# Kernel tuning notes

Measured on AMD Instinct MI355X. Metric: run time of the kernel, lower is better.

The kernel has to match this reference:

```python
import jax, jax.numpy as jnp
import numpy as np

B, T, D_MODEL = 2, 2048, 2048
NUM_HEADS, NUM_KV_HEADS, HEAD_DIM = 16, 16, 128
NUM_Q_HEADS = 2 * NUM_HEADS  # diff-v2 doubles the query heads


def _rope_freqs(seqlen, dim_half, base=10000.0):
    inv = 1.0 / (base ** (np.arange(0, dim_half, dtype=np.float32) / dim_half))
    t = np.arange(seqlen, dtype=np.float32)
    ang = np.outer(t, inv)  # [T, dim_half]
    return jnp.asarray(np.cos(ang)), jnp.asarray(np.sin(ang))


def apply_rotary_interleaved(x, cos, sin):
    # x: [B, T, H, D]; cos/sin: [T, D//2]; pairs are adjacent (interleaved=True)
    x1, x2 = x[..., 0::2], x[..., 1::2]
    c = cos[None, :, None, :]
    s = sin[None, :, None, :]
    o1 = x1 * c - x2 * s
    o2 = x1 * s + x2 * c
    return jnp.stack([o1, o2], axis=-1).reshape(x.shape)


def setup_inputs() -> dict:
    key = jax.random.key(0)
    ks = jax.random.split(key, 6)
    x = jax.random.normal(ks[0], (B, T, D_MODEL), dtype=jnp.float32)
    cos, sin = _rope_freqs(T, HEAD_DIM // 2)
    sc = 1.0 / np.sqrt(D_MODEL)
    Wq = jax.random.normal(ks[1], (D_MODEL, NUM_Q_HEADS * HEAD_DIM), dtype=jnp.float32) * sc
    Wk = jax.random.normal(ks[2], (D_MODEL, NUM_KV_HEADS * HEAD_DIM), dtype=jnp.float32) * sc
    Wv = jax.random.normal(ks[3], (D_MODEL, NUM_KV_HEADS * HEAD_DIM), dtype=jnp.float32) * sc
    Wo = jax.random.normal(ks[4], (NUM_HEADS * HEAD_DIM, D_MODEL), dtype=jnp.float32) * sc
    Wlam = jax.random.normal(ks[5], (D_MODEL, NUM_HEADS), dtype=jnp.float32) * sc
    return {"x": x, "cos": cos, "sin": sin, "Wq": Wq, "Wk": Wk, "Wv": Wv, "Wo": Wo, "Wlam": Wlam}


def reference(x, cos, sin, Wq, Wk, Wv, Wo, Wlam):
    b, t, _ = x.shape
    q = (x @ Wq).reshape(b, t, NUM_Q_HEADS, HEAD_DIM)
    k = (x @ Wk).reshape(b, t, NUM_KV_HEADS, HEAD_DIM)
    v = (x @ Wv).reshape(b, t, NUM_KV_HEADS, HEAD_DIM)
    q = apply_rotary_interleaved(q, cos, sin)
    k = apply_rotary_interleaved(k, cos, sin)
    # GQA: repeat kv heads to match the doubled query heads
    rep = NUM_Q_HEADS // NUM_KV_HEADS
    k = jnp.repeat(k, rep, axis=2)
    v = jnp.repeat(v, rep, axis=2)
    scale = 1.0 / np.sqrt(HEAD_DIM)
    scores = jnp.einsum('bthd,bshd->bhts', q, k) * scale  # [B, 2H, T, T]
    causal = jnp.tril(jnp.ones((t, t), dtype=bool))
    scores = jnp.where(causal[None, None], scores, jnp.finfo(scores.dtype).min)
    p = jax.nn.softmax(scores, axis=-1)
    attn = jnp.einsum('bhts,bshd->bthd', p, v)  # [B, T, 2H, D]
    lam = jax.nn.sigmoid(x @ Wlam)  # [B, T, H]
    attn1, attn2 = attn[:, :, 0::2], attn[:, :, 1::2]
    out = attn1 - lam[..., None] * attn2  # [B, T, H, D]
    return out.reshape(b, t, NUM_HEADS * HEAD_DIM) @ Wo
```

## Files before the change

kernel.cpp:

```cpp
#include <hip/hip_runtime.h>

#define T_SEQ 2048
#define BATCH 2
#define DMODEL 2048
#define NQH 32
#define NKVH 16
#define HD 128

typedef _Float16 f16;
typedef _Float16 f16x8 __attribute__((ext_vector_type(8)));
typedef _Float16 f16x4 __attribute__((ext_vector_type(4)));
typedef _Float16 f16x2 __attribute__((ext_vector_type(2)));
typedef float f32x4 __attribute__((ext_vector_type(4)));

typedef const __attribute__((address_space(1))) void* gptr_t;
typedef __attribute__((address_space(3))) void* sptr_t;
#define GLDS16(g, l) __builtin_amdgcn_global_load_lds((gptr_t)(g), (sptr_t)(l), 16, 0, 0)

__global__ __launch_bounds__(256) void k_transpose_all(const float* __restrict__ Wq,
                                                       const float* __restrict__ Wk,
                                                       const float* __restrict__ Wv,
                                                       const float* __restrict__ Wo,
                                                       f16* __restrict__ WqkvT,
                                                       f16* __restrict__ WoT) {
  __shared__ float tile[32][33];
  const int z = blockIdx.z;
  const float* W;
  f16* WT;
  int N;
  if (z == 0)      { W = Wq; WT = WqkvT;                          N = 4096; }
  else if (z == 1) { W = Wk; WT = WqkvT + (size_t)4096 * 2048;    N = 2048; }
  else if (z == 2) { W = Wv; WT = WqkvT + (size_t)6144 * 2048;    N = 2048; }
  else             { W = Wo; WT = WoT;                            N = 2048; }
  const int K = 2048;
  int n0 = blockIdx.x * 32;
  if (n0 >= N) return;
  int k0 = blockIdx.y * 32;
  int tx = threadIdx.x & 31;
  int ty0 = threadIdx.x >> 5;
  #pragma unroll
  for (int i = 0; i < 4; ++i) {
    int ty = ty0 + i * 8;
    tile[ty][tx] = W[(size_t)(k0 + ty) * N + n0 + tx];
  }
  __syncthreads();
  #pragma unroll
  for (int i = 0; i < 4; ++i) {
    int ty = ty0 + i * 8;
    WT[(size_t)(n0 + ty) * K + k0 + tx] = (f16)tile[tx][ty];
  }
}

template<int BM, int BN, int WM, int WN, int OM>
__global__ __launch_bounds__(512, 2) void k_gemm2(const f16* __restrict__ A,
                                                  const f16* __restrict__ BT,
                                                  void* __restrict__ C0,
                                                  f16* __restrict__ Kh,
                                                  f16* __restrict__ VTg,
                                                  const float* __restrict__ cosb,
                                                  const float* __restrict__ sinb,
                                                  int M, int N, int K) {
  constexpr int MR = BM / WM / 16;
  constexpr int NR = BN / WN / 16;
  constexpr int ACH = BM / 64;
  constexpr int BCH = BN / 64;
  __shared__ alignas(16) f16 Al[2][BM * 64];
  __shared__ alignas(16) f16 Bl[2][BN * 64];
  const int tid = threadIdx.x;
  const int lane = tid & 63;
  const int w = tid >> 6;
  const int wr = w / WN, wc = w % WN;
  const int lr = lane & 15, lg = lane >> 4;
  const int nbx = N / BN;
  const int cpx = gridDim.x >> 3;
  const int wg = (blockIdx.x & 7) * cpx + (blockIdx.x >> 3);
  const int m0 = (wg / nbx) * BM, n0 = (wg % nbx) * BN;

  auto STAGE = [&](int buf, int kk) {
    #pragma unroll
    for (int q = 0; q < ACH; ++q) {
      int idx = q * 512 + tid;
      int r = idx >> 3, g = idx & 7;
      GLDS16(A + (size_t)(m0 + r) * K + kk + ((g ^ (r & 7)) * 8), &Al[buf][idx * 8]);
    }
    #pragma unroll
    for (int q = 0; q < BCH; ++q) {
      int idx = q * 512 + tid;
      int r = idx >> 3, g = idx & 7;
      GLDS16(BT + (size_t)(n0 + r) * K + kk + ((g ^ (r & 7)) * 8), &Bl[buf][idx * 8]);
    }
  };

  f32x4 acc[MR][NR] = {};
  STAGE(0, 0);
  const int nt = K / 64;
  #pragma unroll 2
  for (int t = 0; t < nt; ++t) {
    const int buf = t & 1;
    if (t + 1 < nt) {
      STAGE(buf ^ 1, (t + 1) * 64);
      __builtin_amdgcn_sched_barrier(0);
      if constexpr (ACH + BCH == 8) asm volatile("s_waitcnt vmcnt(8)" ::: "memory");
      else                          asm volatile("s_waitcnt vmcnt(6)" ::: "memory");
    } else {
      __builtin_amdgcn_sched_barrier(0);
      asm volatile("s_waitcnt vmcnt(0)" ::: "memory");
    }
    __builtin_amdgcn_s_barrier();
    __builtin_amdgcn_sched_barrier(0);
    #pragma unroll
    for (int kh = 0; kh < 2; ++kh) {
      f16x8 af[MR], bf[NR];
      #pragma unroll
      for (int i = 0; i < MR; ++i) {
        int r = wr * (BM / WM) + i * 16 + lr;
        af[i] = *(const f16x8*)&Al[buf][r * 64 + (((kh * 4 + lg) ^ (r & 7)) * 8)];
      }
      #pragma unroll
      for (int j = 0; j < NR; ++j) {
        int r = wc * (BN / WN) + j * 16 + lr;
        bf[j] = *(const f16x8*)&Bl[buf][r * 64 + (((kh * 4 + lg) ^ (r & 7)) * 8)];
      }
      #pragma unroll
      for (int i = 0; i < MR; ++i)
        #pragma unroll
        for (int j = 0; j < NR; ++j)
          acc[i][j] = __builtin_amdgcn_mfma_f32_16x16x32_f16(af[i], bf[j], acc[i][j], 0, 0, 0);
    }
    __builtin_amdgcn_sched_barrier(0);
    __builtin_amdgcn_s_barrier();
    __builtin_amdgcn_sched_barrier(0);
  }

  const int mb = m0 + wr * (BM / WM);
  const int nb = n0 + wc * (BN / WN);
  if constexpr (OM == 0) {
    float* C = (float*)C0;
    #pragma unroll
    for (int i = 0; i < MR; ++i)
      #pragma unroll
      for (int j = 0; j < NR; ++j) {
        int r0 = mb + i * 16 + lg * 4;
        int c = nb + j * 16 + lr;
        #pragma unroll
        for (int r = 0; r < 4; ++r)
          C[(size_t)(r0 + r) * N + c] = acc[i][j][r];
      }
  } else {
    if (n0 < 6144) {
      f16* dst = (n0 < 4096) ? (f16*)C0 : Kh;
      const int ncols = (n0 < 4096) ? 4096 : 2048;
      const int coff = (n0 < 4096) ? 0 : 4096;
      #pragma unroll
      for (int i = 0; i < MR; ++i)
        #pragma unroll
        for (int j = 0; j < NR; ++j) {
          int c = nb + j * 16 + lr - coff;
          int jp = (c & 127) >> 1;
          bool odd = (c & 1);
          #pragma unroll
          for (int r = 0; r < 4; ++r) {
            int row = mb + i * 16 + lg * 4 + r;
            int t = row & (T_SEQ - 1);
            float v = acc[i][j][r];
            float pv = __shfl_xor(v, 1);
            float cs = cosb[t * 64 + jp], sn = sinb[t * 64 + jp];
            float out = odd ? (pv * sn + v * cs) : (v * cs - pv * sn);
            dst[(size_t)row * ncols + c] = (f16)out;
          }
        }
    } else {
      #pragma unroll
      for (int i = 0; i < MR; ++i)
        #pragma unroll
        for (int j = 0; j < NR; ++j) {
          int c = nb + j * 16 + lr - 6144;
          int head = c >> 7, d = c & 127;
          int row0 = mb + i * 16 + lg * 4;
          int bb = row0 >> 11, t0 = row0 & (T_SEQ - 1);
          f16x4 zv;
          #pragma unroll
          for (int r = 0; r < 4; ++r) zv[r] = (f16)acc[i][j][r];
          *(f16x4*)(VTg + ((size_t)(bb * NKVH + head) * HD + d) * T_SEQ + t0) = zv;
        }
    }
  }
}

__global__ __launch_bounds__(256) void k_lambda_conv(const float* __restrict__ x,
                                                     const float* __restrict__ Wlam,
                                                     float* __restrict__ lam,
                                                     f16* __restrict__ xh) {
  int row = blockIdx.x;
  const float* xr = x + (size_t)row * DMODEL;
  const int e = threadIdx.x * 8;
  const float4* xp = (const float4*)(xr + e);
  float4 a = xp[0], b2 = xp[1];
  float xv[8] = {a.x, a.y, a.z, a.w, b2.x, b2.y, b2.z, b2.w};
  f16x8 hv;
  #pragma unroll
  for (int j = 0; j < 8; ++j) hv[j] = (f16)xv[j];
  *(f16x8*)(xh + (size_t)row * DMODEL + e) = hv;
  float acc[16];
  #pragma unroll
  for (int h = 0; h < 16; ++h) acc[h] = 0.f;
  #pragma unroll
  for (int j = 0; j < 8; ++j) {
    const float4* wp = (const float4*)(Wlam + (size_t)(e + j) * 16);
    #pragma unroll
    for (int g = 0; g < 4; ++g) {
      float4 wv = wp[g];
      acc[g * 4 + 0] += xv[j] * wv.x; acc[g * 4 + 1] += xv[j] * wv.y;
      acc[g * 4 + 2] += xv[j] * wv.z; acc[g * 4 + 3] += xv[j] * wv.w;
    }
  }
  #pragma unroll
  for (int h = 0; h < 16; ++h)
    for (int off = 32; off > 0; off >>= 1)
      acc[h] += __shfl_down(acc[h], off);
  __shared__ float part[4][16];
  int lane = threadIdx.x & 63, w = threadIdx.x >> 6;
  if (lane == 0) {
    #pragma unroll
    for (int h = 0; h < 16; ++h) part[w][h] = acc[h];
  }
  __syncthreads();
  if (threadIdx.x < 16) {
    float s = part[0][threadIdx.x] + part[1][threadIdx.x] + part[2][threadIdx.x] + part[3][threadIdx.x];
    lam[row * 16 + threadIdx.x] = 1.f / (1.f + __expf(-s));
  }
}

__global__ __launch_bounds__(512, 4) void k_attn5(const f16* __restrict__ Q,
                                                  const f16* __restrict__ K,
                                                  const f16* __restrict__ VT,
                                                  f16* __restrict__ O) {
  __shared__ f16 Kl[64 * 128];
  __shared__ f16 Vl[128 * 64];
  __shared__ f16 Pl[8][16][40];
  const int tid = threadIdx.x;
  const int lane = tid & 63;
  const int w = tid >> 6;
  const int lr = lane & 15, lg = lane >> 4;
  const int flat = blockIdx.x;
  const int xcd = flat & 7;
  const int work = xcd * 64 + (flat >> 3);
  const int grp = work >> 4;
  const int bx = work & 15;
  const int b = grp >> 4, hkv = grp & 15;
  const int h = hkv * 2 + (w >> 2);
  const int wq = w & 3;
  const int kvstride = NKVH * HD;
  const f16* Kg  = K  + (size_t)b * T_SEQ * kvstride + hkv * HD;
  const f16* VTg = VT + (size_t)(b * NKVH + hkv) * HD * T_SEQ;
  const float sc = 0.08838834764831845f;

  #pragma unroll 1
  for (int half = 0; half < 2; ++half) {
    const int qt = half ? (31 - bx) : bx;
    const int qb = qt * 64;
    const int qw = qb + wq * 16;
    const int qrow = qw + lr;
    f16x8 qf[4];
    {
      const f16* qp = Q + (size_t)(b * T_SEQ + qrow) * (NQH * HD) + h * HD + lg * 8;
      #pragma unroll
      for (int c = 0; c < 4; ++c) qf[c] = *(const f16x8*)(qp + c * 32);
    }
    f32x4 o[8] = {};
    float mi = -1e30f, li = 0.f;

    const int nt = qt + 1;
    #pragma unroll
    for (int q = 0; q < 2; ++q) {
      int idx = q * 512 + tid;
      int r = idx >> 4, g = idx & 15;
      GLDS16(Kg + (size_t)r * kvstride + (g ^ (r & 7)) * 8, &Kl[idx * 8]);
    }
    #pragma unroll
    for (int q = 0; q < 2; ++q) {
      int idx = q * 512 + tid;
      int d = idx >> 3, g = idx & 7;
      GLDS16(VTg + (size_t)d * T_SEQ + (g ^ (d & 7)) * 8, &Vl[idx * 8]);
    }
    __syncthreads();

    #pragma unroll 1
    for (int t = 0; t < nt; ++t) {
      const int s0 = t * 64;
      const bool pf = (t + 1 < nt);
      f16x8 ka[2], va[2];
      if (pf) {
        const int s1 = s0 + 64;
        #pragma unroll
        for (int q = 0; q < 2; ++q) {
          int idx = q * 512 + tid;
          int r = idx >> 4, g = idx & 15;
          ka[q] = *(const f16x8*)(Kg + (size_t)(s1 + r) * kvstride + g * 8);
        }
        #pragma unroll
        for (int q = 0; q < 2; ++q) {
          int idx = q * 512 + tid;
          int d = idx >> 3, g = idx & 7;
          va[q] = *(const f16x8*)(VTg + (size_t)d * T_SEQ + s1 + g * 8);
        }
      }
      f32x4 sf[4] = {};
      __builtin_amdgcn_s_setprio(1);
      #pragma unroll
      for (int c = 0; c < 4; ++c) {
        #pragma unroll
        for (int nb = 0; nb < 4; ++nb) {
          f16x8 kf = *(const f16x8*)&Kl[(((nb * 16 + lr) * 16) + ((c * 4 + lg) ^ (lr & 7))) * 8];
          sf[nb] = __builtin_amdgcn_mfma_f32_16x16x32_f16(kf, qf[c], sf[nb], 0, 0, 0);
        }
      }
      __builtin_amdgcn_s_setprio(0);
      float v[16];
      #pragma unroll
      for (int nb = 0; nb < 4; ++nb)
        #pragma unroll
        for (int rr = 0; rr < 4; ++rr) {
          float x = sf[nb][rr] * sc;
          int kv = s0 + nb * 4 * 4 + nb * 0 + nb * 0;
          kv = s0 + nb * 16 + lg * 4 + rr;
          v[nb * 4 + rr] = (kv > qrow) ? -1e30f : x;
        }
      float pm = v[0];
      #pragma unroll
      for (int i = 1; i < 16; ++i) pm = fmaxf(pm, v[i]);
      pm = fmaxf(pm, __shfl_xor(pm, 16));
      pm = fmaxf(pm, __shfl_xor(pm, 32));
      const bool nogrow = (__all(pm <= mi + 8.0f) != 0);
      const float mnew = nogrow ? mi : fmaxf(mi, pm);
      float rs = 0.f;
      #pragma unroll
      for (int i = 0; i < 16; ++i) { float p = __expf(v[i] - mnew); v[i] = p; rs += p; }
      rs += __shfl_xor(rs, 16);
      rs += __shfl_xor(rs, 32);
      if (nogrow) {
        li += rs;
      } else {
        float a = __expf(mi - mnew);
        mi = mnew;
        li = a * li + rs;
        float ab[4];
        #pragma unroll
        for (int rr = 0; rr < 4; ++rr) ab[rr] = __shfl(a, lg * 4 + rr);
        #pragma unroll
        for (int j = 0; j < 8; ++j)
          #pragma unroll
          for (int rr = 0; rr < 4; ++rr) o[j][rr] *= ab[rr];
      }
      #pragma unroll
      for (int ks = 0; ks < 2; ++ks) {
        #pragma unroll
        for (int nb2 = 0; nb2 < 2; ++nb2) {
          int nb = ks * 2 + nb2;
          f16x4 pk;
          #pragma unroll
          for (int rr = 0; rr < 4; ++rr) pk[rr] = (f16)v[nb * 4 + rr];
          *(f16x4*)&Pl[w][lr][nb2 * 16 + lg * 4] = pk;
        }
        f16x8 pa = *(const f16x8*)&Pl[w][lr][lg * 8];
        __builtin_amdgcn_s_setprio(1);
        #pragma unroll
        for (int j = 0; j < 8; ++j) {
          f16x8 vbj = *(const f16x8*)&Vl[(((j * 16 + lr) * 8) + ((ks * 4 + lg) ^ (lr & 7))) * 8];
          o[j] = __builtin_amdgcn_mfma_f32_16x16x32_f16(pa, vbj, o[j], 0, 0, 0);
        }
        __builtin_amdgcn_s_setprio(0);
      }
      __syncthreads();
      if (pf) {
        #pragma unroll
        for (int q = 0; q < 2; ++q) {
          int idx = q * 512 + tid;
          int r = idx >> 4, g = idx & 15;
          *(f16x8*)&Kl[(r * 16 + (g ^ (r & 7))) * 8] = ka[q];
        }
        #pragma unroll
        for (int q = 0; q < 2; ++q) {
          int idx = q * 512 + tid;
          int d = idx >> 3, g = idx & 7;
          *(f16x8*)&Vl[(d * 8 + (g ^ (d & 7))) * 8] = va[q];
        }
      }
      __syncthreads();
    }
    float lib[4];
    #pragma unroll
    for (int rr = 0; rr < 4; ++rr) lib[rr] = 1.f / __shfl(li, lg * 4 + rr);
    #pragma unroll
    for (int j = 0; j < 8; ++j)
      #pragma unroll
      for (int rr = 0; rr < 4; ++rr) {
        float vv = o[j][rr] * lib[rr];
        O[(size_t)(b * T_SEQ + qw + lg * 4 + rr) * (NQH * HD) + h * HD + j * 16 + lr] = (f16)vv;
      }
  }
}

__global__ void k_combine(const f16* __restrict__ attn, const float* __restrict__ lam,
                          f16* __restrict__ Z) {
  int idx = blockIdx.x * blockDim.x + threadIdx.x;
  int d4 = idx & 31;
  int tmp = idx >> 5;
  int h = tmp & 15;
  int row = tmp >> 4;
  if (row >= BATCH * T_SEQ) return;
  float lv = lam[row * 16 + h];
  f16x4 a1 = *(const f16x4*)(attn + (size_t)row * 4096 + (2 * h) * 128 + d4 * 4);
  f16x4 a2 = *(const f16x4*)(attn + (size_t)row * 4096 + (2 * h + 1) * 128 + d4 * 4);
  f16x4 z;
  #pragma unroll
  for (int e = 0; e < 4; ++e) z[e] = (f16)((float)a1[e] - lv * (float)a2[e]);
  *(f16x4*)(Z + (size_t)row * 2048 + h * 128 + d4 * 4) = z;
}

extern "C" void kernel_launch(void* const* d_in, const int* in_sizes, int n_in,
                              void* d_out, int out_size, void* d_ws, size_t ws_size,
                              hipStream_t stream) {
  const float* x    = (const float*)d_in[0];
  const float* cosb = (const float*)d_in[1];
  const float* sinb = (const float*)d_in[2];
  const float* Wq   = (const float*)d_in[3];
  const float* Wk   = (const float*)d_in[4];
  const float* Wv   = (const float*)d_in[5];
  const float* Wo   = (const float*)d_in[6];
  const float* Wlam = (const float*)d_in[7];

  char* ws = (char*)d_ws;
  f16*  xh     = (f16*)(ws);
  f16*  WqkvT  = (f16*)(ws + 16777216);
  f16*  WoT    = (f16*)(ws + 50331648);
  f16*  Qh     = (f16*)(ws + 58720256);
  f16*  Kh     = (f16*)(ws + 92274688);
  f16*  VTg    = (f16*)(ws + 109051904);
  f16*  At     = (f16*)(ws + 125829120);
  f16*  Zh     = (f16*)(ws + 159383552);
  float* lam   = (float*)(ws + 176160768);

  k_transpose_all<<<dim3(128, 64, 4), 256, 0, stream>>>(Wq, Wk, Wv, Wo, WqkvT, WoT);
  k_lambda_conv<<<4096, 256, 0, stream>>>(x, Wlam, lam, xh);

  k_gemm2<256, 256, 2, 4, 3><<<512, 512, 0, stream>>>(xh, WqkvT, Qh, Kh, VTg,
                                                      cosb, sinb, 4096, 8192, 2048);

  k_attn5<<<512, 512, 0, stream>>>(Qh, Kh, VTg, At);

  k_combine<<<(BATCH * T_SEQ * 16 * 32) / 256, 256, 0, stream>>>(At, lam, Zh);

  k_gemm2<256, 128, 4, 2, 0><<<256, 512, 0, stream>>>(Zh, WoT, d_out, nullptr, nullptr,
                                                      nullptr, nullptr, 4096, 2048, 2048);
}
```

Before: 439.8 us.

## Fuse lambda combine into attention epilogue and retile output projection GEMM

The attention kernel now pairs the two query heads of each KV group inside one block. The odd head's normalized output is written to shared memory and the even-head waves compute attn1 - lam*attn2, writing Z directly. This removes the separate combine kernel and the round trip of the full 2H attention tensor through global memory, at the cost of extra LDS and a block barrier. The output projection GEMM is also retuned to 128x128 tiles with 256 threads and 512 blocks, using a templated thread count to fill more CUs.

```diff
diff --git a/kernel.cpp b/kernel.cpp
--- a/kernel.cpp
+++ b/kernel.cpp
@@ -51,19 +51,20 @@
   }
 }
 
-template<int BM, int BN, int WM, int WN, int OM>
-__global__ __launch_bounds__(512, 2) void k_gemm2(const f16* __restrict__ A,
-                                                  const f16* __restrict__ BT,
-                                                  void* __restrict__ C0,
-                                                  f16* __restrict__ Kh,
-                                                  f16* __restrict__ VTg,
-                                                  const float* __restrict__ cosb,
-                                                  const float* __restrict__ sinb,
-                                                  int M, int N, int K) {
+template<int BM, int BN, int WM, int WN, int THREADS, int OM>
+__global__ __launch_bounds__(THREADS, 2) void k_gemm2(const f16* __restrict__ A,
+                                                      const f16* __restrict__ BT,
+                                                      void* __restrict__ C0,
+                                                      f16* __restrict__ Kh,
+                                                      f16* __restrict__ VTg,
+                                                      const float* __restrict__ cosb,
+                                                      const float* __restrict__ sinb,
+                                                      int M, int N, int K) {
   constexpr int MR = BM / WM / 16;
   constexpr int NR = BN / WN / 16;
-  constexpr int ACH = BM / 64;
-  constexpr int BCH = BN / 64;
+  constexpr int ACH = BM * 64 / 8 / THREADS;
+  constexpr int BCH = BN * 64 / 8 / THREADS;
+  static_assert(ACH + BCH == 8, "vmcnt constant assumes 8 loads/thread/stage");
   __shared__ alignas(16) f16 Al[2][BM * 64];
   __shared__ alignas(16) f16 Bl[2][BN * 64];
   const int tid = threadIdx.x;
@@ -79,13 +80,13 @@
   auto STAGE = [&](int buf, int kk) {
     #pragma unroll
     for (int q = 0; q < ACH; ++q) {
-      int idx = q * 512 + tid;
+      int idx = q * THREADS + tid;
       int r = idx >> 3, g = idx & 7;
       GLDS16(A + (size_t)(m0 + r) * K + kk + ((g ^ (r & 7)) * 8), &Al[buf][idx * 8]);
     }
     #pragma unroll
     for (int q = 0; q < BCH; ++q) {
-      int idx = q * 512 + tid;
+      int idx = q * THREADS + tid;
       int r = idx >> 3, g = idx & 7;
       GLDS16(BT + (size_t)(n0 + r) * K + kk + ((g ^ (r & 7)) * 8), &Bl[buf][idx * 8]);
     }
@@ -100,8 +101,7 @@
     if (t + 1 < nt) {
       STAGE(buf ^ 1, (t + 1) * 64);
       __builtin_amdgcn_sched_barrier(0);
-      if constexpr (ACH + BCH == 8) asm volatile("s_waitcnt vmcnt(8)" ::: "memory");
-      else                          asm volatile("s_waitcnt vmcnt(6)" ::: "memory");
+      asm volatile("s_waitcnt vmcnt(8)" ::: "memory");
     } else {
       __builtin_amdgcn_sched_barrier(0);
       asm volatile("s_waitcnt vmcnt(0)" ::: "memory");
@@ -231,13 +231,15 @@
   }
 }
 
-__global__ __launch_bounds__(512, 4) void k_attn5(const f16* __restrict__ Q,
+__global__ __launch_bounds__(512, 4) void k_attn6(const f16* __restrict__ Q,
                                                   const f16* __restrict__ K,
                                                   const f16* __restrict__ VT,
-                                                  f16* __restrict__ O) {
+                                                  const float* __restrict__ lam,
+                                                  f16* __restrict__ Z) {
   __shared__ f16 Kl[64 * 128];
   __shared__ f16 Vl[128 * 64];
   __shared__ f16 Pl[8][16][40];
+  __shared__ f16 Po[4][16][136];
   const int tid = threadIdx.x;
   const int lane = tid & 63;
   const int w = tid >> 6;
@@ -322,8 +324,7 @@
         #pragma unroll
         for (int rr = 0; rr < 4; ++rr) {
           float x = sf[nb][rr] * sc;
-          int kv = s0 + nb * 4 * 4 + nb * 0 + nb * 0;
-          kv = s0 + nb * 16 + lg * 4 + rr;
+          int kv = s0 + nb * 16 + lg * 4 + rr;
           v[nb * 4 + rr] = (kv > qrow) ? -1e30f : x;
         }
       float pm = v[0];
@@ -391,31 +392,31 @@
     float lib[4];
     #pragma unroll
     for (int rr = 0; rr < 4; ++rr) lib[rr] = 1.f / __shfl(li, lg * 4 + rr);
-    #pragma unroll
-    for (int j = 0; j < 8; ++j)
-      #pragma unroll
-      for (int rr = 0; rr < 4; ++rr) {
-        float vv = o[j][rr] * lib[rr];
-        O[(size_t)(b * T_SEQ + qw + lg * 4 + rr) * (NQH * HD) + h * HD + j * 16 + lr] = (f16)vv;
-      }
-  }
-}
-
-__global__ void k_combine(const f16* __restrict__ attn, const float* __restrict__ lam,
-                          f16* __restrict__ Z) {
-  int idx = blockIdx.x * blockDim.x + threadIdx.x;
-  int d4 = idx & 31;
-  int tmp = idx >> 5;
-  int h = tmp & 15;
-  int row = tmp >> 4;
-  if (row >= BATCH * T_SEQ) return;
-  float lv = lam[row * 16 + h];
-  f16x4 a1 = *(const f16x4*)(attn + (size_t)row * 4096 + (2 * h) * 128 + d4 * 4);
-  f16x4 a2 = *(const f16x4*)(attn + (size_t)row * 4096 + (2 * h + 1) * 128 + d4 * 4);
-  f16x4 z;
-  #pragma unroll
-  for (int e = 0; e < 4; ++e) z[e] = (f16)((float)a1[e] - lv * (float)a2[e]);
-  *(f16x4*)(Z + (size_t)row * 2048 + h * 128 + d4 * 4) = z;
+    if (w >= 4) {
+      #pragma unroll
+      for (int j = 0; j < 8; ++j)
+        #pragma unroll
+        for (int rr = 0; rr < 4; ++rr)
+          Po[wq][lg * 4 + rr][j * 16 + lr] = (f16)(o[j][rr] * lib[rr]);
+    }
+    __syncthreads();
+    if (w < 4) {
+      float lamv[4];
+      #pragma unroll
+      for (int rr = 0; rr < 4; ++rr)
+        lamv[rr] = lam[(size_t)(b * T_SEQ + qw + lg * 4 + rr) * 16 + hkv];
+      #pragma unroll
+      for (int j = 0; j < 8; ++j)
+        #pragma unroll
+        for (int rr = 0; rr < 4; ++rr) {
+          float a1 = o[j][rr] * lib[rr];
+          float a2 = (float)Po[wq][lg * 4 + rr][j * 16 + lr];
+          Z[(size_t)(b * T_SEQ + qw + lg * 4 + rr) * 2048 + hkv * 128 + j * 16 + lr] =
+              (f16)(a1 - lamv[rr] * a2);
+        }
+    }
+    __syncthreads();
+  }
 }
 
 extern "C" void kernel_launch(void* const* d_in, const int* in_sizes, int n_in,
@@ -437,20 +438,17 @@
   f16*  Qh     = (f16*)(ws + 58720256);
   f16*  Kh     = (f16*)(ws + 92274688);
   f16*  VTg    = (f16*)(ws + 109051904);
-  f16*  At     = (f16*)(ws + 125829120);
   f16*  Zh     = (f16*)(ws + 159383552);
   float* lam   = (float*)(ws + 176160768);
 
   k_transpose_all<<<dim3(128, 64, 4), 256, 0, stream>>>(Wq, Wk, Wv, Wo, WqkvT, WoT);
   k_lambda_conv<<<4096, 256, 0, stream>>>(x, Wlam, lam, xh);
 
-  k_gemm2<256, 256, 2, 4, 3><<<512, 512, 0, stream>>>(xh, WqkvT, Qh, Kh, VTg,
-                                                      cosb, sinb, 4096, 8192, 2048);
-
-  k_attn5<<<512, 512, 0, stream>>>(Qh, Kh, VTg, At);
-
-  k_combine<<<(BATCH * T_SEQ * 16 * 32) / 256, 256, 0, stream>>>(At, lam, Zh);
-
-  k_gemm2<256, 128, 4, 2, 0><<<256, 512, 0, stream>>>(Zh, WoT, d_out, nullptr, nullptr,
-                                                      nullptr, nullptr, 4096, 2048, 2048);
+  k_gemm2<256, 256, 2, 4, 512, 3><<<512, 512, 0, stream>>>(xh, WqkvT, Qh, Kh, VTg,
+                                                           cosb, sinb, 4096, 8192, 2048);
+
+  k_attn6<<<512, 512, 0, stream>>>(Qh, Kh, VTg, lam, Zh);
+
+  k_gemm2<128, 128, 2, 2, 256, 0><<<512, 256, 0, stream>>>(Zh, WoT, d_out, nullptr, nullptr,
+                                                           nullptr, nullptr, 4096, 2048, 2048);
 }
```

After: 420.7 us. -4.3%, faster.
